# Optimization experiments

Hardware: AMD Instinct MI355X
Metric: run time of the kernel (lower is better)

Reference implementation:

```python
import jax, jax.numpy as jnp
import numpy as np

BS, N, HID = 16384, 16, 512  # batch, n coords (state dim = 2n), mlp hidden


def setup_inputs() -> dict:
    key = jax.random.key(0)
    ks = jax.random.split(key, 4)
    d = 2 * N
    x = jax.random.normal(ks[0], (BS, d), dtype=jnp.float32)
    # Lagrangian MLP: 2n -> HID -> HID -> 1 with softplus (smooth 2nd derivs)
    W1 = jax.random.normal(ks[1], (d, HID), dtype=jnp.float32) / np.sqrt(d)
    b1 = jnp.zeros((HID,), jnp.float32)
    W2 = jax.random.normal(ks[2], (HID, HID), dtype=jnp.float32) / np.sqrt(HID)
    b2 = jnp.zeros((HID,), jnp.float32)
    W3 = jax.random.normal(ks[3], (HID, 1), dtype=jnp.float32) / np.sqrt(HID)
    b3 = jnp.zeros((1,), jnp.float32)
    return {"x": x, "W1": W1, "b1": b1, "W2": W2, "b2": b2, "W3": W3, "b3": b3}


def reference(x, W1, b1, W2, b2, W3, b3):
    n = x.shape[1] // 2

    def lagrangian(qqd):  # qqd: [2n] -> scalar
        h = jax.nn.softplus(qqd @ W1 + b1)
        h = jax.nn.softplus(h @ W2 + b2)
        return jnp.sum(h @ W3 + b3)

    # batched first derivative (jacobian of scalar) and hessian; replaces the
    # per-sample python loop of torch.autograd.functional.jacobian/hessian
    jac = jax.vmap(jax.grad(lagrangian))(x)          # [bs, 2n]
    hess = jax.vmap(jax.hessian(lagrangian))(x)      # [bs, 2n, 2n]

    qd = x[:, n:]                                    # [bs, n]
    A = hess[:, n:, n:]                              # d2L/dqd dqd  [bs, n, n]
    B = hess[:, n:, :n]                              # d2L/dqd dq   [bs, n, n]
    rhs = jac[:, :n] - jnp.einsum('bij,bj->bi', B, qd)  # [bs, n]
    qdd = jnp.einsum('bij,bj->bi', jnp.linalg.pinv(A), rhs)  # [bs, n]
    return jnp.concatenate([qd, qdd], axis=1)        # [bs, 2n]
```

## Files before the change

### kernel.cpp

```cpp
#include <hip/hip_runtime.h>
#include <math.h>


#define NSWEEP 5
#define JAX_RCOND 1.9073486e-5

typedef unsigned int uint;
typedef unsigned short ushort;
typedef float f2 __attribute__((ext_vector_type(2)));
typedef float f4 __attribute__((ext_vector_type(4)));
typedef short bf16x8 __attribute__((ext_vector_type(8)));
typedef float f32x16 __attribute__((ext_vector_type(16)));
typedef uint uint2v __attribute__((ext_vector_type(2)));

#define OFF_R    0
#define R_FLOATS 6144
#define OFF_S1   (OFF_R + R_FLOATS)
#define OFF_H1   (OFF_S1+512)
#define OFF_G2   (OFF_H1+512)
#define OFF_D2   (OFF_G2+512)
#define OFF_U    (OFF_D2+512)
#define OFF_X    (OFF_U+512)
#define OFF_JAC  (OFF_X+32)
#define OFF_T1   (OFF_JAC+16)
#define OFF_T2   (OFF_T1+528)
#define OFF_AUG  (OFF_T2+528)
#define SMEM_FLOATS (OFF_AUG+272)
#define SMEM_BYTES  (SMEM_FLOATS*4)

#define SOLVE_WAVE_DBL 592
#define SOLVE_SMEM_BYTES (4*SOLVE_WAVE_DBL*8)

#define PACK_BYTES 524288

__device__ __forceinline__ ushort f2bf(float x) {
    uint u = __float_as_uint(x);
    return (ushort)((u + 0x7fffu + ((u >> 16) & 1u)) >> 16);
}
__device__ __forceinline__ float bf2f(ushort h) {
    return __uint_as_float(((uint)h) << 16);
}
__device__ __forceinline__ void split3(float x, ushort& h, ushort& m, ushort& l) {
    h = f2bf(x); float r1 = x - bf2f(h);
    m = f2bf(r1); float r2 = r1 - bf2f(m);
    l = f2bf(r2);
}

__device__ __forceinline__ void pairpq(int r, int m, int& p, int& q) {
    p = (m == 0) ? 0 : 1 + (m - 1 + r) % 15;
    q = 1 + (14 - m + r) % 15;
}

__device__ __forceinline__ void wave_fence() {
    __builtin_amdgcn_wave_barrier();
    __builtin_amdgcn_s_waitcnt(0);
    __builtin_amdgcn_wave_barrier();
}

__device__ __forceinline__ void jacobi_solve_wave(
    const float* __restrict__ gaug, double* __restrict__ ws,
    float* __restrict__ outp, int lane)
{
    double* Ad  = ws;
    double* Vd  = Ad + 272;
    double* c8  = Vd + 272;
    double* sn8 = c8 + 8;
    double* il  = sn8 + 8;
    double* yv  = il + 16;

    for (int idx = lane; idx < 272; idx += 64) {
        const int r = idx / 17, c = idx - r*17;
        double a = 0.0;
        if (c < 16) a = 0.5 * ((double)gaug[r*17 + c] + (double)gaug[c*17 + r]);
        Ad[idx] = a;
        Vd[idx] = (c < 16 && r == c) ? 1.0 : 0.0;
    }
    wave_fence();

    for (int sweep = 0; sweep < NSWEEP; ++sweep) {
        for (int rr = 0; rr < 15; ++rr) {
            if (lane < 8) {
                int p, q; pairpq(rr, lane, p, q);
                const double app = Ad[p*17 + p], aqq = Ad[q*17 + q], apq = Ad[p*17 + q];
                double cc = 1.0, ss = 0.0;
                if (apq != 0.0) {
                    const double tau = (aqq - app) / (2.0 * apq);
                    const double tt = ((tau >= 0.0) ? 1.0 : -1.0) / (fabs(tau) + sqrt(1.0 + tau*tau));
                    cc = 1.0 / sqrt(1.0 + tt*tt);
                    ss = tt * cc;
                }
                c8[lane] = cc; sn8[lane] = ss;
            }
            wave_fence();
            #pragma unroll
            for (int k = 0; k < 2; ++k) {
                const int id = lane + 64*k;
                const int m = id >> 4, j = id & 15;
                int p, q; pairpq(rr, m, p, q);
                const double cc = c8[m], ss = sn8[m];
                const double ap = Ad[p*17 + j], aq = Ad[q*17 + j];
                Ad[p*17 + j] = cc*ap - ss*aq;
                Ad[q*17 + j] = ss*ap + cc*aq;
            }
            #pragma unroll
            for (int k = 0; k < 2; ++k) {
                const int id = lane + 64*k;
                const int m = id >> 4, i = id & 15;
                int p, q; pairpq(rr, m, p, q);
                const double cc = c8[m], ss = sn8[m];
                const double vp = Vd[i*17 + p], vq = Vd[i*17 + q];
                Vd[i*17 + p] = cc*vp - ss*vq;
                Vd[i*17 + q] = ss*vp + cc*vq;
            }
            wave_fence();
            #pragma unroll
            for (int k = 0; k < 2; ++k) {
                const int id = lane + 64*k;
                const int m = id >> 4, i = id & 15;
                int p, q; pairpq(rr, m, p, q);
                const double cc = c8[m], ss = sn8[m];
                const double ap = Ad[i*17 + p], aq = Ad[i*17 + q];
                Ad[i*17 + p] = cc*ap - ss*aq;
                Ad[i*17 + q] = ss*ap + cc*aq;
            }
            wave_fence();
        }
    }

    if (lane == 0) {
        double mx = 0.0;
        #pragma unroll
        for (int i = 0; i < 16; ++i) mx = fmax(mx, fabs(Ad[i*17 + i]));
        const double cut = JAX_RCOND * mx;
        #pragma unroll
        for (int i = 0; i < 16; ++i) {
            const double l = Ad[i*17 + i];
            il[i] = (fabs(l) > cut) ? (1.0 / l) : 0.0;
        }
    }
    wave_fence();

    if (lane < 16) {
        double a = 0.0;
        #pragma unroll
        for (int r = 0; r < 16; ++r) a += Vd[r*17 + lane] * (double)gaug[r*17 + 16];
        yv[lane] = a;
    }
    wave_fence();

    if (lane < 16) {
        double a = 0.0;
        #pragma unroll
        for (int i = 0; i < 16; ++i) a += Vd[lane*17 + i] * (il[i] * yv[i]);
        outp[lane] = (float)a;
    }
}

extern "C" __global__ void w1_transpose(const float* __restrict__ W1,
                                        float* __restrict__ W1T) {
    const int t = blockIdx.x * 256 + threadIdx.x;
    W1T[t] = W1[(t & 31) * 512 + (t >> 5)];
}

extern "C" __global__ void w2_pack(const float* __restrict__ W2,
                                   uint* __restrict__ pHi,
                                   uint* __restrict__ pMid,
                                   uint* __restrict__ pLo) {
    const int tid = blockIdx.x * 256 + threadIdx.x;
    const int lane = tid & 63;
    const int k0 = ((tid >> 6) & 31) * 16 + (lane >> 5) * 8;
    const int n  = (tid >> 11) * 32 + (lane & 31);
    uint h[4], m[4], l[4];
    #pragma unroll
    for (int e2 = 0; e2 < 4; ++e2) {
        ushort h0, m0, l0, h1, m1, l1;
        split3(W2[(k0 + 2*e2    )*512 + n], h0, m0, l0);
        split3(W2[(k0 + 2*e2 + 1)*512 + n], h1, m1, l1);
        h[e2] = (uint)h0 | ((uint)h1 << 16);
        m[e2] = (uint)m0 | ((uint)m1 << 16);
        l[e2] = (uint)l0 | ((uint)l1 << 16);
    }
    #pragma unroll
    for (int e2 = 0; e2 < 4; ++e2) {
        pHi [tid*4 + e2] = h[e2];
        pMid[tid*4 + e2] = m[e2];
        pLo [tid*4 + e2] = l[e2];
    }
}

#define MFMA32(A, B, C) __builtin_amdgcn_mfma_f32_32x32x16_bf16((A), (B), (C), 0, 0, 0)

extern "C" __global__ __launch_bounds__(256, 4)
void lnn_kernel(const float* __restrict__ x,
                const float* __restrict__ W1,
                const float* __restrict__ W1T,
                const float* __restrict__ b1,
                const float* __restrict__ W2, const float* __restrict__ b2,
                const float* __restrict__ W3,
                float* __restrict__ out,
                float* __restrict__ aug_g,
                const uint* __restrict__ pHi,
                const uint* __restrict__ pMid,
                const uint* __restrict__ pLo,
                const int solveInMain)
{
    const int b = blockIdx.x;
    const int t = threadIdx.x;
    const int lane = t & 63;
    const int w = t >> 6;

    extern __shared__ float sm[];
    char*  A8    = (char*)sm;
    float* s_ws  = sm + OFF_R;
    char*  Mq8   = (char*)sm;
    float* s_s1  = sm + OFF_S1;
    float* s_h1  = sm + OFF_H1;
    float* s_g2  = sm + OFF_G2;
    float* s_d2  = sm + OFF_D2;
    float* s_u   = sm + OFF_U;
    float* s_x   = sm + OFF_X;
    float* s_jac = sm + OFF_JAC;
    float* s_T1  = sm + OFF_T1;
    float* s_T2  = sm + OFF_T2;
    float* s_aug = sm + OFF_AUG;

    if (t < 32) s_x[t] = x[b*32 + t];
    if (t < 16) out[b*32 + t] = x[b*32 + 16 + t];
    __syncthreads();

    #pragma unroll
    for (int rep = 0; rep < 2; ++rep) {
        const int j = t + rep*256;
        float z = b1[j];
        #pragma unroll
        for (int i = 0; i < 32; ++i) z = fmaf(s_x[i], W1[i*512 + j], z);
        const float e = expf(-fabsf(z));
        const float s = (z >= 0.f) ? 1.f/(1.f+e) : e/(1.f+e);
        s_s1[j] = s;
        s_h1[j] = fmaxf(z, 0.f) + log1pf(e);
    }
    __syncthreads();

    {
        const int c = w*128 + lane*2;
        const f2 bz = *(const f2*)(b2 + c);
        float za0 = bz.x, za1 = bz.y;
        #pragma unroll 16
        for (int j = 0; j < 512; ++j) {
            const f2 wv = *(const f2*)(W2 + j*512 + c);
            const float h = s_h1[j];
            za0 = fmaf(h, wv.x, za0);
            za1 = fmaf(h, wv.y, za1);
        }
        const f2 w3v = *(const f2*)(W3 + c);
        const float e0 = expf(-fabsf(za0));
        const float sg0 = (za0 >= 0.f) ? 1.f/(1.f+e0) : e0/(1.f+e0);
        const float e1v = expf(-fabsf(za1));
        const float sg1 = (za1 >= 0.f) ? 1.f/(1.f+e1v) : e1v/(1.f+e1v);
        f2 g2v = { w3v.x * sg0, w3v.y * sg1 };
        f2 d2v = { w3v.x * sg0 * (1.f - sg0), w3v.y * sg1 * (1.f - sg1) };
        *(f2*)(s_g2 + c) = g2v;
        *(f2*)(s_d2 + c) = d2v;
    }
    __syncthreads();

    {
        float g2f[8];
        {
            const float4 ga = *(const float4*)(s_g2 + lane*8);
            const float4 gb = *(const float4*)(s_g2 + lane*8 + 4);
            g2f[0]=ga.x; g2f[1]=ga.y; g2f[2]=ga.z; g2f[3]=ga.w;
            g2f[4]=gb.x; g2f[5]=gb.y; g2f[6]=gb.z; g2f[7]=gb.w;
        }
        for (int jj = 0; jj < 32; ++jj) {
            float pr[4];
            #pragma unroll
            for (int s = 0; s < 4; ++s) {
                const int j = w*128 + jj + s*32;
                const float4 ra = *(const float4*)(W2 + j*512 + lane*8);
                const float4 rb = *(const float4*)(W2 + j*512 + lane*8 + 4);
                float p0 = ra.x*g2f[0];
                p0 = fmaf(ra.y, g2f[1], p0); p0 = fmaf(ra.z, g2f[2], p0); p0 = fmaf(ra.w, g2f[3], p0);
                p0 = fmaf(rb.x, g2f[4], p0); p0 = fmaf(rb.y, g2f[5], p0);
                p0 = fmaf(rb.z, g2f[6], p0); p0 = fmaf(rb.w, g2f[7], p0);
                pr[s] = p0;
            }
            #pragma unroll
            for (int off = 32; off >= 1; off >>= 1) {
                #pragma unroll
                for (int s = 0; s < 4; ++s) pr[s] += __shfl_xor(pr[s], off);
            }
            if (lane == 0) {
                #pragma unroll
                for (int s = 0; s < 4; ++s) s_u[w*128 + jj + s*32] = pr[s];
            }
        }
    }
    __syncthreads();

    #pragma unroll
    for (int rep = 0; rep < 2; ++rep) {
        const int j = t + rep*256;
        const float uj = s_u[j], s = s_s1[j];
        s_h1[j] = uj * (1.f - s) / s;
    }

    const int i5 = 16 + (t >> 4);
    const int c5 = 2 * (t & 15);

    {
        const f4* W1Tv4 = (const f4*)W1T;
        float jacp = 0.f, t1a = 0.f, t1b = 0.f;

        for (int q = 0; q < 4; ++q) {
            __syncthreads();
            #pragma unroll
            for (int r = 0; r < 4; ++r) {
                const int f = r*256 + t;
                f4 v = W1Tv4[q*1024 + f];
                const float s = s_s1[q*128 + (f >> 3)];
                v.x*=s; v.y*=s; v.z*=s; v.w*=s;
                ((f4*)s_ws)[f] = v;
            }
            __syncthreads();

            if (w == q) {
                const int i  = t & 15;
                const int jb = (lane >> 4) * 32;
                #pragma unroll 8
                for (int jj = 0; jj < 32; ++jj)
                    jacp = fmaf(s_ws[(jb+jj)*32 + i], s_u[q*128 + jb + jj], jacp);
            }

            #pragma unroll 4
            for (int jj = 0; jj < 128; ++jj) {
                const float e   = s_h1[q*128 + jj];
                const float wsi = s_ws[jj*32 + i5];
                const f2 wc = *(const f2*)(s_ws + jj*32 + c5);
                const float tt  = wsi * e;
                t1a = fmaf(tt, wc.x, t1a);
                t1b = fmaf(tt, wc.y, t1b);
            }
        }
        s_T1[(i5-16)*33 + c5]     = t1a;
        s_T1[(i5-16)*33 + c5 + 1] = t1b;
        s_g2[(t>>4)*16 + (t&15)]  = jacp;
    }
    __syncthreads();

    if (t < 16) {
        float p = 0.f;
        #pragma unroll
        for (int seg = 0; seg < 16; ++seg) p += s_g2[seg*16 + t];
        s_jac[t] = p;
    }

    float h0 = 0.f, h1v = 0.f;
    {
        const f4* W1v4 = (const f4*)W1;
        const f4* s1v4 = (const f4*)s_s1;
        const bf16x8* pHiV  = (const bf16x8*)pHi;
        const bf16x8* pMidV = (const bf16x8*)pMid;
        const bf16x8* pLoV  = (const bf16x8*)pLo;
        const int arow = lane & 31;
        const uint abase = (uint)arow * 256u;
        const uint aswz = (uint)(arow & 15);
        const f4* d2q = (const f4*)s_d2;
        const int rowadd = 4 * (lane >> 5);
        const int cl = lane & 31;
        const uint swi = (uint)((i5 >> 1) & 7);
        const uint swc = (uint)((c5 >> 1) & 7);
        char* MiB = Mq8 + i5*528;
        char* MaB = Mq8 + c5*528;
        char* MbB = Mq8 + (c5+1)*528;

        #pragma unroll 1
        for (int half = 0; half < 2; ++half) {
            f32x16 acc0{}, acc1{};
            const int NT0 = 2*half, NT1 = 2*half + 1;

            #pragma unroll 1
            for (int q = 0; q < 4; ++q) {
                __syncthreads();
                #pragma unroll
                for (int r = 0; r < 4; ++r) {
                    const int f = r*256 + t;
                    const int i = f >> 5, k4 = f & 31;
                    const f4 wv = W1v4[i*128 + q*32 + k4];
                    const f4 sv = s1v4[q*32 + k4];
                    ushort h[4], m[4], l[4];
                    split3(wv.x*sv.x, h[0], m[0], l[0]);
                    split3(wv.y*sv.y, h[1], m[1], l[1]);
                    split3(wv.z*sv.z, h[2], m[2], l[2]);
                    split3(wv.w*sv.w, h[3], m[3], l[3]);
                    const uint off = (uint)i*256u + (((uint)k4*8u) ^ (((uint)(i & 15)) << 4));
                    uint2v vh = { (uint)h[0] | ((uint)h[1]<<16), (uint)h[2] | ((uint)h[3]<<16) };
                    uint2v vm = { (uint)m[0] | ((uint)m[1]<<16), (uint)m[2] | ((uint)m[3]<<16) };
                    uint2v vl = { (uint)l[0] | ((uint)l[1]<<16), (uint)l[2] | ((uint)l[3]<<16) };
                    *(uint2v*)(A8 + off)         = vh;
                    *(uint2v*)(A8 + 8192 + off)  = vm;
                    *(uint2v*)(A8 + 16384 + off) = vl;
                }
                __syncthreads();

                #pragma unroll 2
                for (int ks8 = 0; ks8 < 8; ++ks8) {
                    const uint slot = (uint)(ks8*2 + (lane >> 5));
                    const uint aoff = abase + ((slot ^ aswz) << 4);
                    const bf16x8 aHi  = *(const bf16x8*)(A8 + aoff);
                    const bf16x8 aMid = *(const bf16x8*)(A8 + 8192 + aoff);
                    const bf16x8 aLo  = *(const bf16x8*)(A8 + 16384 + aoff);
                    const int pbase = (w*128 + q*8 + ks8)*64 + lane;
                    #define KSTEP(ACC, NT) { \
                        const bf16x8 bHi  = pHiV [pbase + (NT)*2048]; \
                        const bf16x8 bMid = pMidV[pbase + (NT)*2048]; \
                        const bf16x8 bLo  = pLoV [pbase + (NT)*2048]; \
                        ACC = MFMA32(aHi,  bHi,  ACC); \
                        ACC = MFMA32(aHi,  bMid, ACC); \
                        ACC = MFMA32(aMid, bHi,  ACC); \
                        ACC = MFMA32(aMid, bMid, ACC); \
                        ACC = MFMA32(aHi,  bLo,  ACC); \
                        ACC = MFMA32(aLo,  bHi,  ACC); }
                    KSTEP(acc0, NT0)
                    KSTEP(acc1, NT1)
                    #undef KSTEP
                }
            }
            __syncthreads();

            for (int p = 0; p < 4; ++p) {
                if (w == p) {
                    #define WRFRAG(ACC, NT) { \
                        _Pragma("unroll") \
                        for (int r = 0; r < 16; ++r) { \
                            const int row = (r & 3) + 8*(r >> 2) + rowadd; \
                            const int col = (NT)*32 + cl; \
                            const uint slot = ((uint)(col >> 2)) ^ ((uint)((row >> 1) & 7)); \
                            *(float*)(Mq8 + row*528 + (slot << 4) + ((col & 3) << 2)) = ACC[r]; \
                        } }
                    WRFRAG(acc0, NT0)
                    WRFRAG(acc1, NT1)
                    #undef WRFRAG
                }
                __syncthreads();
                for (int qq = half*16; qq < half*16 + 16; ++qq) {
                    const f4 d  = d2q[p*32 + qq];
                    const f4 mi = *(const f4*)(MiB + (((uint)qq ^ swi) << 4));
                    const f4 ma = *(const f4*)(MaB + (((uint)qq ^ swc) << 4));
                    const f4 mb = *(const f4*)(MbB + (((uint)qq ^ swc) << 4));
                    float tt;
                    tt = mi.x*d.x; h0 = fmaf(tt, ma.x, h0); h1v = fmaf(tt, mb.x, h1v);
                    tt = mi.y*d.y; h0 = fmaf(tt, ma.y, h0); h1v = fmaf(tt, mb.y, h1v);
                    tt = mi.z*d.z; h0 = fmaf(tt, ma.z, h0); h1v = fmaf(tt, mb.z, h1v);
                    tt = mi.w*d.w; h0 = fmaf(tt, ma.w, h0); h1v = fmaf(tt, mb.w, h1v);
                }
                __syncthreads();
            }
        }
        s_T2[(i5-16)*33 + c5]     = h0;
        s_T2[(i5-16)*33 + c5 + 1] = h1v;
    }
    __syncthreads();

    {
        const int r = t >> 4, c = t & 15;
        s_aug[r*17 + c] = s_T1[r*33 + 16 + c] + s_T2[r*33 + 16 + c];
    }
    if (t < 16) {
        float p = s_jac[t];
        #pragma unroll
        for (int c = 0; c < 16; ++c)
            p -= (s_T1[t*33 + c] + s_T2[t*33 + c]) * s_x[16 + c];
        s_aug[t*17 + 16] = p;
    }
    __syncthreads();

    if (!solveInMain) {
        aug_g[b*272 + t] = s_aug[t];
        if (t < 16) aug_g[b*272 + 256 + t] = s_aug[256 + t];
        return;
    }

    if (w != 0) return;
    jacobi_solve_wave(s_aug, (double*)sm, out + b*32 + 16, lane);
}

extern "C" __global__ __launch_bounds__(256, 8)
void lnn_solve(const float* __restrict__ aug_g, float* __restrict__ out)
{
    const int t = threadIdx.x;
    const int lane = t & 63;
    const int w = t >> 6;
    const int b = blockIdx.x * 4 + w;

    extern __shared__ double dsm[];
    jacobi_solve_wave(aug_g + b*272, dsm + w*SOLVE_WAVE_DBL, out + b*32 + 16, lane);
}

extern "C" void kernel_launch(void* const* d_in, const int* in_sizes, int n_in,
                              void* d_out, int out_size, void* d_ws, size_t ws_size,
                              hipStream_t stream) {
    const float* x  = (const float*)d_in[0];
    const float* W1 = (const float*)d_in[1];
    const float* b1 = (const float*)d_in[2];
    const float* W2 = (const float*)d_in[3];
    const float* b2 = (const float*)d_in[4];
    const float* W3 = (const float*)d_in[5];
    float* out = (float*)d_out;

    float* W1T = (float*)d_ws;
    uint*  pHi  = (uint*)((char*)d_ws + 65536);
    uint*  pMid = (uint*)((char*)d_ws + 65536 + PACK_BYTES);
    uint*  pLo  = (uint*)((char*)d_ws + 65536 + 2*PACK_BYTES);
    float* aug  = (float*)((char*)d_ws + 65536 + 3*PACK_BYTES);
    const int bs = in_sizes[0] / 32;

    const size_t need = 65536 + 3*(size_t)PACK_BYTES + (size_t)bs * 272 * 4;
    const int solveInMain = (ws_size < need) ? 1 : 0;

    hipFuncSetAttribute((const void*)lnn_kernel,
                        hipFuncAttributeMaxDynamicSharedMemorySize, SMEM_BYTES);
    w1_transpose<<<dim3(64), dim3(256), 0, stream>>>(W1, W1T);
    w2_pack<<<dim3(128), dim3(256), 0, stream>>>(W2, pHi, pMid, pLo);
    lnn_kernel<<<dim3(bs), dim3(256), SMEM_BYTES, stream>>>(
        x, W1, W1T, b1, W2, b2, W3, out, aug, pHi, pMid, pLo, solveInMain);
    if (!solveInMain)
        lnn_solve<<<dim3(bs/4), dim3(256), SOLVE_SMEM_BYTES, stream>>>(aug, out);
}
```

Before: 3.655 ms.

## Fold layer-2 forward matvec into the split-bf16 MFMA Hessian loop

The forward layer-2 preactivation h1·W2 is now computed inside the existing MFMA loop, using an extra accumulator fed with a split-bf16 broadcast of h1 and the W2 B-fragments that are already loaded. This removes the separate fp32 scalar pass that streamed all of W2 from global memory for every sample. Softplus derivatives g2 and d2 are produced per half right after the MFMA loop, and the backward g2·W2ᵀ and T1 stages are moved after the Hessian contraction. The cost is twice as many MFMA instructions, where the new accumulator uses only one of its 32 rows. The inner-loop unroll is also lowered from 2 to 1.

```diff
diff --git a/kernel.cpp b/kernel.cpp
--- a/kernel.cpp
+++ b/kernel.cpp
@@ -223,6 +223,9 @@
     float* s_T1  = sm + OFF_T1;
     float* s_T2  = sm + OFF_T2;
     float* s_aug = sm + OFF_AUG;
+    char*  zHiB = (char*)s_u;
+    char*  zMidB = (char*)s_u + 1024;
+    char*  zLoB  = (char*)s_h1;
 
     if (t < 32) s_x[t] = x[b*32 + t];
     if (t < 16) out[b*32 + t] = x[b*32 + 16 + t];
@@ -242,120 +245,20 @@
     __syncthreads();
 
     {
-        const int c = w*128 + lane*2;
-        const f2 bz = *(const f2*)(b2 + c);
-        float za0 = bz.x, za1 = bz.y;
-        #pragma unroll 16
-        for (int j = 0; j < 512; ++j) {
-            const f2 wv = *(const f2*)(W2 + j*512 + c);
-            const float h = s_h1[j];
-            za0 = fmaf(h, wv.x, za0);
-            za1 = fmaf(h, wv.y, za1);
-        }
-        const f2 w3v = *(const f2*)(W3 + c);
-        const float e0 = expf(-fabsf(za0));
-        const float sg0 = (za0 >= 0.f) ? 1.f/(1.f+e0) : e0/(1.f+e0);
-        const float e1v = expf(-fabsf(za1));
-        const float sg1 = (za1 >= 0.f) ? 1.f/(1.f+e1v) : e1v/(1.f+e1v);
-        f2 g2v = { w3v.x * sg0, w3v.y * sg1 };
-        f2 d2v = { w3v.x * sg0 * (1.f - sg0), w3v.y * sg1 * (1.f - sg1) };
-        *(f2*)(s_g2 + c) = g2v;
-        *(f2*)(s_d2 + c) = d2v;
-    }
-    __syncthreads();
-
-    {
-        float g2f[8];
-        {
-            const float4 ga = *(const float4*)(s_g2 + lane*8);
-            const float4 gb = *(const float4*)(s_g2 + lane*8 + 4);
-            g2f[0]=ga.x; g2f[1]=ga.y; g2f[2]=ga.z; g2f[3]=ga.w;
-            g2f[4]=gb.x; g2f[5]=gb.y; g2f[6]=gb.z; g2f[7]=gb.w;
-        }
-        for (int jj = 0; jj < 32; ++jj) {
-            float pr[4];
-            #pragma unroll
-            for (int s = 0; s < 4; ++s) {
-                const int j = w*128 + jj + s*32;
-                const float4 ra = *(const float4*)(W2 + j*512 + lane*8);
-                const float4 rb = *(const float4*)(W2 + j*512 + lane*8 + 4);
-                float p0 = ra.x*g2f[0];
-                p0 = fmaf(ra.y, g2f[1], p0); p0 = fmaf(ra.z, g2f[2], p0); p0 = fmaf(ra.w, g2f[3], p0);
-                p0 = fmaf(rb.x, g2f[4], p0); p0 = fmaf(rb.y, g2f[5], p0);
-                p0 = fmaf(rb.z, g2f[6], p0); p0 = fmaf(rb.w, g2f[7], p0);
-                pr[s] = p0;
-            }
-            #pragma unroll
-            for (int off = 32; off >= 1; off >>= 1) {
-                #pragma unroll
-                for (int s = 0; s < 4; ++s) pr[s] += __shfl_xor(pr[s], off);
-            }
-            if (lane == 0) {
-                #pragma unroll
-                for (int s = 0; s < 4; ++s) s_u[w*128 + jj + s*32] = pr[s];
-            }
-        }
-    }
-    __syncthreads();
-
-    #pragma unroll
-    for (int rep = 0; rep < 2; ++rep) {
-        const int j = t + rep*256;
-        const float uj = s_u[j], s = s_s1[j];
-        s_h1[j] = uj * (1.f - s) / s;
+        const float a = s_h1[2*t], c = s_h1[2*t + 1];
+        __syncthreads();
+        ushort ha, ma, la, hc, mc, lc;
+        split3(a, ha, ma, la);
+        split3(c, hc, mc, lc);
+        ((uint*)zHiB)[t]  = (uint)ha | ((uint)hc << 16);
+        ((uint*)zMidB)[t] = (uint)ma | ((uint)mc << 16);
+        ((uint*)zLoB)[t]  = (uint)la | ((uint)lc << 16);
     }
 
     const int i5 = 16 + (t >> 4);
     const int c5 = 2 * (t & 15);
 
-    {
-        const f4* W1Tv4 = (const f4*)W1T;
-        float jacp = 0.f, t1a = 0.f, t1b = 0.f;
-
-        for (int q = 0; q < 4; ++q) {
-            __syncthreads();
-            #pragma unroll
-            for (int r = 0; r < 4; ++r) {
-                const int f = r*256 + t;
-                f4 v = W1Tv4[q*1024 + f];
-                const float s = s_s1[q*128 + (f >> 3)];
-                v.x*=s; v.y*=s; v.z*=s; v.w*=s;
-                ((f4*)s_ws)[f] = v;
-            }
-            __syncthreads();
-
-            if (w == q) {
-                const int i  = t & 15;
-                const int jb = (lane >> 4) * 32;
-                #pragma unroll 8
-                for (int jj = 0; jj < 32; ++jj)
-                    jacp = fmaf(s_ws[(jb+jj)*32 + i], s_u[q*128 + jb + jj], jacp);
-            }
-
-            #pragma unroll 4
-            for (int jj = 0; jj < 128; ++jj) {
-                const float e   = s_h1[q*128 + jj];
-                const float wsi = s_ws[jj*32 + i5];
-                const f2 wc = *(const f2*)(s_ws + jj*32 + c5);
-                const float tt  = wsi * e;
-                t1a = fmaf(tt, wc.x, t1a);
-                t1b = fmaf(tt, wc.y, t1b);
-            }
-        }
-        s_T1[(i5-16)*33 + c5]     = t1a;
-        s_T1[(i5-16)*33 + c5 + 1] = t1b;
-        s_g2[(t>>4)*16 + (t&15)]  = jacp;
-    }
-    __syncthreads();
-
-    if (t < 16) {
-        float p = 0.f;
-        #pragma unroll
-        for (int seg = 0; seg < 16; ++seg) p += s_g2[seg*16 + t];
-        s_jac[t] = p;
-    }
-
-    float h0 = 0.f, h1v = 0.f;
+    float h0acc = 0.f, h1acc = 0.f;
     {
         const f4* W1v4 = (const f4*)W1;
         const f4* s1v4 = (const f4*)s_s1;
@@ -365,6 +268,7 @@
         const int arow = lane & 31;
         const uint abase = (uint)arow * 256u;
         const uint aswz = (uint)(arow & 15);
+        const uint kbyte = (uint)((lane >> 5) << 4);
         const f4* d2q = (const f4*)s_d2;
         const int rowadd = 4 * (lane >> 5);
         const int cl = lane & 31;
@@ -376,7 +280,7 @@
 
         #pragma unroll 1
         for (int half = 0; half < 2; ++half) {
-            f32x16 acc0{}, acc1{};
+            f32x16 acc0{}, acc1{}, az0{}, az1{};
             const int NT0 = 2*half, NT1 = 2*half + 1;
 
             #pragma unroll 1
@@ -403,15 +307,19 @@
                 }
                 __syncthreads();
 
-                #pragma unroll 2
+                #pragma unroll 1
                 for (int ks8 = 0; ks8 < 8; ++ks8) {
                     const uint slot = (uint)(ks8*2 + (lane >> 5));
                     const uint aoff = abase + ((slot ^ aswz) << 4);
                     const bf16x8 aHi  = *(const bf16x8*)(A8 + aoff);
                     const bf16x8 aMid = *(const bf16x8*)(A8 + 8192 + aoff);
                     const bf16x8 aLo  = *(const bf16x8*)(A8 + 16384 + aoff);
+                    const uint zoff = (uint)(q*256 + ks8*32) + kbyte;
+                    const bf16x8 zHi  = *(const bf16x8*)(zHiB + zoff);
+                    const bf16x8 zMid = *(const bf16x8*)(zMidB + zoff);
+                    const bf16x8 zLo  = *(const bf16x8*)(zLoB + zoff);
                     const int pbase = (w*128 + q*8 + ks8)*64 + lane;
-                    #define KSTEP(ACC, NT) { \
+                    #define KSTEP(ACC, AZ, NT) { \
                         const bf16x8 bHi  = pHiV [pbase + (NT)*2048]; \
                         const bf16x8 bMid = pMidV[pbase + (NT)*2048]; \
                         const bf16x8 bLo  = pLoV [pbase + (NT)*2048]; \
@@ -420,11 +328,33 @@
                         ACC = MFMA32(aMid, bHi,  ACC); \
                         ACC = MFMA32(aMid, bMid, ACC); \
                         ACC = MFMA32(aHi,  bLo,  ACC); \
-                        ACC = MFMA32(aLo,  bHi,  ACC); }
-                    KSTEP(acc0, NT0)
-                    KSTEP(acc1, NT1)
+                        ACC = MFMA32(aLo,  bHi,  ACC); \
+                        AZ  = MFMA32(zHi,  bHi,  AZ); \
+                        AZ  = MFMA32(zHi,  bMid, AZ); \
+                        AZ  = MFMA32(zMid, bHi,  AZ); \
+                        AZ  = MFMA32(zMid, bMid, AZ); \
+                        AZ  = MFMA32(zHi,  bLo,  AZ); \
+                        AZ  = MFMA32(zLo,  bHi,  AZ); }
+                    KSTEP(acc0, az0, NT0)
+                    KSTEP(acc1, az1, NT1)
                     #undef KSTEP
                 }
+            }
+
+            if (lane < 32) {
+                const int c0g = w*128 + NT0*32 + lane;
+                const int c1g = c0g + 32;
+                const float z0 = az0[0] + b2[c0g];
+                const float z1 = az1[0] + b2[c1g];
+                const float e0 = expf(-fabsf(z0));
+                const float sg0 = (z0 >= 0.f) ? 1.f/(1.f+e0) : e0/(1.f+e0);
+                const float e1v = expf(-fabsf(z1));
+                const float sg1 = (z1 >= 0.f) ? 1.f/(1.f+e1v) : e1v/(1.f+e1v);
+                const float w30 = W3[c0g], w31 = W3[c1g];
+                s_g2[c0g] = w30 * sg0;
+                s_d2[c0g] = w30 * sg0 * (1.f - sg0);
+                s_g2[c1g] = w31 * sg1;
+                s_d2[c1g] = w31 * sg1 * (1.f - sg1);
             }
             __syncthreads();
 
@@ -449,23 +379,112 @@
                     const f4 ma = *(const f4*)(MaB + (((uint)qq ^ swc) << 4));
                     const f4 mb = *(const f4*)(MbB + (((uint)qq ^ swc) << 4));
                     float tt;
-                    tt = mi.x*d.x; h0 = fmaf(tt, ma.x, h0); h1v = fmaf(tt, mb.x, h1v);
-                    tt = mi.y*d.y; h0 = fmaf(tt, ma.y, h0); h1v = fmaf(tt, mb.y, h1v);
-                    tt = mi.z*d.z; h0 = fmaf(tt, ma.z, h0); h1v = fmaf(tt, mb.z, h1v);
-                    tt = mi.w*d.w; h0 = fmaf(tt, ma.w, h0); h1v = fmaf(tt, mb.w, h1v);
+                    tt = mi.x*d.x; h0acc = fmaf(tt, ma.x, h0acc); h1acc = fmaf(tt, mb.x, h1acc);
+                    tt = mi.y*d.y; h0acc = fmaf(tt, ma.y, h0acc); h1acc = fmaf(tt, mb.y, h1acc);
+                    tt = mi.z*d.z; h0acc = fmaf(tt, ma.z, h0acc); h1acc = fmaf(tt, mb.z, h1acc);
+                    tt = mi.w*d.w; h0acc = fmaf(tt, ma.w, h0acc); h1acc = fmaf(tt, mb.w, h1acc);
                 }
                 __syncthreads();
             }
         }
-        s_T2[(i5-16)*33 + c5]     = h0;
-        s_T2[(i5-16)*33 + c5 + 1] = h1v;
-    }
-    __syncthreads();
-
+        s_T2[(i5-16)*33 + c5]     = h0acc;
+        s_T2[(i5-16)*33 + c5 + 1] = h1acc;
+    }
+    __syncthreads();
+
+    {
+        float g2f[8];
+        {
+            const float4 ga = *(const float4*)(s_g2 + lane*8);
+            const float4 gb = *(const float4*)(s_g2 + lane*8 + 4);
+            g2f[0]=ga.x; g2f[1]=ga.y; g2f[2]=ga.z; g2f[3]=ga.w;
+            g2f[4]=gb.x; g2f[5]=gb.y; g2f[6]=gb.z; g2f[7]=gb.w;
+        }
+        for (int jj = 0; jj < 32; ++jj) {
+            float pr[4];
+            #pragma unroll
+            for (int s = 0; s < 4; ++s) {
+                const int j = w*128 + jj + s*32;
+                const float4 ra = *(const float4*)(W2 + j*512 + lane*8);
+                const float4 rb = *(const float4*)(W2 + j*512 + lane*8 + 4);
+                float p0 = ra.x*g2f[0];
+                p0 = fmaf(ra.y, g2f[1], p0); p0 = fmaf(ra.z, g2f[2], p0); p0 = fmaf(ra.w, g2f[3], p0);
+                p0 = fmaf(rb.x, g2f[4], p0); p0 = fmaf(rb.y, g2f[5], p0);
+                p0 = fmaf(rb.z, g2f[6], p0); p0 = fmaf(rb.w, g2f[7], p0);
+                pr[s] = p0;
+            }
+            #pragma unroll
+            for (int off = 32; off >= 1; off >>= 1) {
+                #pragma unroll
+                for (int s = 0; s < 4; ++s) pr[s] += __shfl_xor(pr[s], off);
+            }
+            if (lane == 0) {
+                #pragma unroll
+                for (int s = 0; s < 4; ++s) s_u[w*128 + jj + s*32] = pr[s];
+            }
+        }
+    }
+    __syncthreads();
+
+    #pragma unroll
+    for (int rep = 0; rep < 2; ++rep) {
+        const int j = t + rep*256;
+        const float uj = s_u[j], s = s_s1[j];
+        s_h1[j] = uj * (1.f - s) / s;
+    }
+
+    {
+        const f4* W1Tv4 = (const f4*)W1T;
+        float jacp = 0.f, t1a = 0.f, t1b = 0.f;
+
+        for (int q = 0; q < 4; ++q) {
+            __syncthreads();
+            #pragma unroll
+            for (int r = 0; r < 4; ++r) {
+                const int f = r*256 + t;
+                f4 v = W1Tv4[q*1024 + f];
+                const float s = s_s1[q*128 + (f >> 3)];
+                v.x*=s; v.y*=s; v.z*=s; v.w*=s;
+                ((f4*)s_ws)[f] = v;
+            }
+            __syncthreads();
+
+            if (w == q) {
+                const int i  = t & 15;
+                const int jb = (lane >> 4) * 32;
+                #pragma unroll 8
+                for (int jj = 0; jj < 32; ++jj)
+                    jacp = fmaf(s_ws[(jb+jj)*32 + i], s_u[q*128 + jb + jj], jacp);
+            }
+
+            #pragma unroll 4
+            for (int jj = 0; jj < 128; ++jj) {
+                const float e   = s_h1[q*128 + jj];
+                const float wsi = s_ws[jj*32 + i5];
+                const f2 wc = *(const f2*)(s_ws + jj*32 + c5);
+                const float tt  = wsi * e;
+                t1a = fmaf(tt, wc.x, t1a);
+                t1b = fmaf(tt, wc.y, t1b);
+            }
+        }
+        s_T1[(i5-16)*33 + c5]     = t1a;
+        s_T1[(i5-16)*33 + c5 + 1] = t1b;
+        s_g2[(t>>4)*16 + (t&15)]  = jacp;
+    }
+    __syncthreads();
+
+    if (t < 16) {
+        float p = 0.f;
+        #pragma unroll
+        for (int seg = 0; seg < 16; ++seg) p += s_g2[seg*16 + t];
+        s_jac[t] = p;
+    }
     {
         const int r = t >> 4, c = t & 15;
         s_aug[r*17 + c] = s_T1[r*33 + 16 + c] + s_T2[r*33 + 16 + c];
     }
+    __syncthreads();
+
     if (t < 16) {
         float p = s_jac[t];
         #pragma unroll
```

Result: slower. 4.100 ms (+12.2%).
